# Performance work log

Measured on AMD Instinct MI355X. Metric: run time of the kernel, lower is better.

## Reference

```python
import jax, jax.numpy as jnp
import numpy as np

B, L = 8192, 2048

def setup_inputs() -> dict:
    key = jax.random.key(0)
    k1, k2 = jax.random.split(key)
    x = jax.random.normal(k1, (B, L), dtype=jnp.float32)
    y = jax.random.normal(k2, (B, L), dtype=jnp.float32)
    # MRS ppm axis is descending; GABA/Glx windows lie inside [1, 5] ppm
    ppm = jnp.linspace(5.0, 1.0, L, dtype=jnp.float32)
    return {"x": x, "ppm": ppm, "y": y}

def _bounds(ppm_np, lo, hi):
    # matches torch: start = amin(where(ppm <= hi)), stop = amax(where(ppm >= lo))
    mn = int(np.min(np.where(ppm_np <= hi)[0]))
    mx = int(np.max(np.where(ppm_np >= lo)[0]))
    return mn, mx

def _norm01(v):
    vmin = v.min(axis=-1, keepdims=True)
    vmax = v.max(axis=-1, keepdims=True)
    return (v - vmin) / (vmax - vmin)

def _pearson(a, b):
    # row-wise Pearson correlation == corrcoef(cat([a,b]))[0,1], batched over rows
    am = a - a.mean(axis=-1, keepdims=True)
    bm = b - b.mean(axis=-1, keepdims=True)
    return (am * bm).sum(-1) / jnp.sqrt((am * am).sum(-1) * (bm * bm).sum(-1))

def _loss(x, y, ppm_np):
    # ---- ShapeScoreLoss (gaba 2.8-3.2, glx 3.6-3.9, weights 0.6/0.4) ----
    g_lo, g_hi = _bounds(ppm_np, 2.8, 3.2)
    gaba_score = _pearson(_norm01(x[:, g_lo:g_hi]), _norm01(y[:, g_lo:g_hi]))
    s_lo, s_hi = _bounds(ppm_np, 3.6, 3.9)
    glx_score = _pearson(_norm01(x[:, s_lo:s_hi]), _norm01(y[:, s_lo:s_hi]))
    shape_loss = 1.0 - (0.6 * gaba_score + 0.4 * glx_score).mean()
    # ---- RangeMAELoss (gaba 2.8-3.2, glx 3.55-3.95, weights 6/3/1 over 10) ----
    r_lo, r_hi = _bounds(ppm_np, 3.55, 3.95)
    gaba_mae = jnp.abs(x[:, g_lo:g_hi] - y[:, g_lo:g_hi]).mean()
    glx_mae = jnp.abs(x[:, r_lo:r_hi] - y[:, r_lo:r_hi]).mean()
    global_mae = jnp.abs(x - y).mean()
    range_loss = (gaba_mae * 6.0 + glx_mae * 3.0 + global_mae) / 10.0
    return shape_loss + range_loss * 0.5

def reference(x, ppm, y):
    ppm_np = np.asarray(ppm)  # ppm is a fixed axis -> static slice bounds
    return _loss(x, y, ppm_np)
```

## Files before the change

### kernel.cpp

```cpp
#include <hip/hip_runtime.h>

#define L_COLS 2048

typedef float vf4 __attribute__((ext_vector_type(4)));

__device__ __forceinline__ float wave_red(float v) {
#pragma unroll
    for (int m = 32; m >= 1; m >>= 1) v += __shfl_xor(v, m, 64);
    return v;
}

__global__ __launch_bounds__(64) void init_kernel(const float* __restrict__ ppm,
                                                  float* __restrict__ acc,
                                                  int* __restrict__ ob) {
    const int lane = threadIdx.x;
    if (lane < 4) acc[lane] = 0.f;

    int mn0 = 0x7fffffff, mn1 = 0x7fffffff, mn2 = 0x7fffffff;
    int mx0 = -1, mx1 = -1, mx2 = -1;
    const vf4* __restrict__ p4 = (const vf4*)ppm;
#pragma unroll
    for (int k = 0; k < L_COLS / 256; ++k) {
        const int j = k * 64 + lane;
        const vf4 pv = p4[j];
        const float ps[4] = {pv.x, pv.y, pv.z, pv.w};
#pragma unroll
        for (int e = 0; e < 4; ++e) {
            const int c = 4 * j + e;
            const float p = ps[e];
            if (p <= 3.2f)  mn0 = min(mn0, c);
            if (p >= 2.8f)  mx0 = max(mx0, c);
            if (p <= 3.9f)  mn1 = min(mn1, c);
            if (p >= 3.6f)  mx1 = max(mx1, c);
            if (p <= 3.95f) mn2 = min(mn2, c);
            if (p >= 3.55f) mx2 = max(mx2, c);
        }
    }
#pragma unroll
    for (int m = 32; m >= 1; m >>= 1) {
        mn0 = min(mn0, __shfl_xor(mn0, m, 64));
        mx0 = max(mx0, __shfl_xor(mx0, m, 64));
        mn1 = min(mn1, __shfl_xor(mn1, m, 64));
        mx1 = max(mx1, __shfl_xor(mx1, m, 64));
        mn2 = min(mn2, __shfl_xor(mn2, m, 64));
        mx2 = max(mx2, __shfl_xor(mx2, m, 64));
    }
    if (lane == 0) {
        ob[0] = mn0; ob[1] = mx0;
        ob[2] = mn1; ob[3] = mx1;
        ob[4] = mn2; ob[5] = mx2;
    }
}

__global__ __launch_bounds__(256, 2) void loss_main(const float* __restrict__ x,
                                                    const float* __restrict__ y,
                                                    const int* __restrict__ ob,
                                                    float* __restrict__ acc) {
    const int lane = threadIdx.x & 63;
    const int wv   = threadIdx.x >> 6;
    const long row = (long)blockIdx.x * 4 + wv;

    const int g_lo = ob[0], g_hi = ob[1];
    const int s_lo = ob[2], s_hi = ob[3];
    const int r_lo = ob[4], r_hi = ob[5];
    const int lo_any = min(min(g_lo, s_lo), r_lo);
    const int hi_any = max(max(g_hi, s_hi), r_hi);

    const vf4* __restrict__ x4 = (const vf4*)(x + row * L_COLS);
    const vf4* __restrict__ y4 = (const vf4*)(y + row * L_COLS);

    vf4 xr[8], yr[8];
#pragma unroll
    for (int k = 0; k < 8; ++k) xr[k] = x4[k * 64 + lane];
#pragma unroll
    for (int k = 0; k < 8; ++k) yr[k] = y4[k * 64 + lane];

    float gl = 0.f;
    float a_sx = 0, a_sy = 0, a_xy = 0, a_xx = 0, a_yy = 0, a_mae = 0;
    float b_sx = 0, b_sy = 0, b_xy = 0, b_xx = 0, b_yy = 0;
    float r_mae = 0;

#pragma unroll
    for (int k = 0; k < 8; ++k) {
        const vf4 xv = xr[k];
        const vf4 yv = yr[k];
        const float d0 = fabsf(xv.x - yv.x), d1 = fabsf(xv.y - yv.y);
        const float d2 = fabsf(xv.z - yv.z), d3 = fabsf(xv.w - yv.w);
        gl += (d0 + d1) + (d2 + d3);

        if (k * 256 < hi_any && k * 256 + 256 > lo_any) {
            const float xs[4] = {xv.x, xv.y, xv.z, xv.w};
            const float ys[4] = {yv.x, yv.y, yv.z, yv.w};
            const float ds[4] = {d0, d1, d2, d3};
#pragma unroll
            for (int e = 0; e < 4; ++e) {
                const int c = k * 256 + 4 * lane + e;
                const float xe = xs[e], ye = ys[e];
                if (c >= g_lo && c < g_hi) {
                    a_sx += xe; a_sy += ye; a_xy += xe * ye;
                    a_xx += xe * xe; a_yy += ye * ye; a_mae += ds[e];
                }
                if (c >= s_lo && c < s_hi) {
                    b_sx += xe; b_sy += ye; b_xy += xe * ye;
                    b_xx += xe * xe; b_yy += ye * ye;
                }
                if (c >= r_lo && c < r_hi) r_mae += ds[e];
            }
        }
    }

    gl    = wave_red(gl);
    a_sx  = wave_red(a_sx);  a_sy = wave_red(a_sy);
    a_xy  = wave_red(a_xy);  a_xx = wave_red(a_xx);  a_yy = wave_red(a_yy);
    a_mae = wave_red(a_mae);
    b_sx  = wave_red(b_sx);  b_sy = wave_red(b_sy);
    b_xy  = wave_red(b_xy);  b_xx = wave_red(b_xx);  b_yy = wave_red(b_yy);
    r_mae = wave_red(r_mae);

    __shared__ float part[4][4];
    if (lane == 0) {
        const float ng = (float)(g_hi - g_lo);
        const float ns = (float)(s_hi - s_lo);
        const float covA = a_xy - a_sx * a_sy / ng;
        const float vAx  = a_xx - a_sx * a_sx / ng;
        const float vAy  = a_yy - a_sy * a_sy / ng;
        const float scoreA = covA * rsqrtf(vAx * vAy);
        const float covB = b_xy - b_sx * b_sy / ns;
        const float vBx  = b_xx - b_sx * b_sx / ns;
        const float vBy  = b_yy - b_sy * b_sy / ns;
        const float scoreB = covB * rsqrtf(vBx * vBy);
        part[wv][0] = 0.6f * scoreA + 0.4f * scoreB;
        part[wv][1] = a_mae;
        part[wv][2] = r_mae;
        part[wv][3] = gl;
    }
    __syncthreads();
    if (threadIdx.x < 4) {
        const float s = part[0][threadIdx.x] + part[1][threadIdx.x] +
                        part[2][threadIdx.x] + part[3][threadIdx.x];
        atomicAdd(&acc[threadIdx.x], s);
    }
}

__global__ void finalize_kernel(const float* __restrict__ acc, const int* __restrict__ ob,
                                int Brows, float* __restrict__ out) {
    const float ng = (float)(ob[1] - ob[0]);
    const float nr = (float)(ob[5] - ob[4]);
    const float Bf = (float)Brows;
    const float shape_loss = 1.f - acc[0] / Bf;
    const float gaba_mae = acc[1] / (Bf * ng);
    const float glx_mae  = acc[2] / (Bf * nr);
    const float glob_mae = acc[3] / (Bf * (float)L_COLS);
    const float range_loss = (gaba_mae * 6.f + glx_mae * 3.f + glob_mae) * 0.1f;
    out[0] = shape_loss + range_loss * 0.5f;
}

extern "C" void kernel_launch(void* const* d_in, const int* in_sizes, int n_in,
                              void* d_out, int out_size, void* d_ws, size_t ws_size,
                              hipStream_t stream) {
    const float* x   = (const float*)d_in[0];
    const float* ppm = (const float*)d_in[1];
    const float* y   = (const float*)d_in[2];
    const int L = in_sizes[1];
    const int Brows = in_sizes[0] / L;

    float* acc = (float*)d_ws;
    int*   ob  = (int*)((char*)d_ws + 64);

    init_kernel<<<1, 64, 0, stream>>>(ppm, acc, ob);
    loss_main<<<Brows / 4, 256, 0, stream>>>(x, y, ob, acc);
    finalize_kernel<<<1, 1, 0, stream>>>(acc, ob, Brows, (float*)d_out);
}
```

Baseline: 46.50 us.

## Process one row per block and spread atomics over multiple slots

Each row is now handled by a whole 256-thread block, with two vf4 loads per thread instead of one wave loading sixteen, and partial sums are combined through shared memory before the Pearson score is computed once per row. Atomic accumulation goes to 64 separate slot sets chosen by block index, and the finalize kernel reduces those slots with a wave. The aim is more memory parallelism, lower register pressure and less atomic contention. In exchange the grid has four times as many blocks, every thread evaluates the range predicates since the chunk-skip test is gone, and each block now pays a barrier and a serial single-thread final combine.

```diff
diff --git a/kernel.cpp b/kernel.cpp
--- a/kernel.cpp
+++ b/kernel.cpp
@@ -1,6 +1,7 @@
 #include <hip/hip_runtime.h>
 
 #define L_COLS 2048
+#define NSLOT 64
 
 typedef float vf4 __attribute__((ext_vector_type(4)));
 
@@ -14,7 +15,7 @@
                                                   float* __restrict__ acc,
                                                   int* __restrict__ ob) {
     const int lane = threadIdx.x;
-    if (lane < 4) acc[lane] = 0.f;
+    ((vf4*)acc)[lane] = (vf4){0.f, 0.f, 0.f, 0.f};
 
     int mn0 = 0x7fffffff, mn1 = 0x7fffffff, mn2 = 0x7fffffff;
     int mx0 = -1, mx1 = -1, mx2 = -1;
@@ -52,28 +53,26 @@
     }
 }
 
-__global__ __launch_bounds__(256, 2) void loss_main(const float* __restrict__ x,
-                                                    const float* __restrict__ y,
-                                                    const int* __restrict__ ob,
-                                                    float* __restrict__ acc) {
-    const int lane = threadIdx.x & 63;
-    const int wv   = threadIdx.x >> 6;
-    const long row = (long)blockIdx.x * 4 + wv;
+__global__ __launch_bounds__(256) void loss_main(const float* __restrict__ x,
+                                                 const float* __restrict__ y,
+                                                 const int* __restrict__ ob,
+                                                 float* __restrict__ acc) {
+    const int t    = threadIdx.x;
+    const int lane = t & 63;
+    const int wv   = t >> 6;
+    const long row = blockIdx.x;
 
     const int g_lo = ob[0], g_hi = ob[1];
     const int s_lo = ob[2], s_hi = ob[3];
     const int r_lo = ob[4], r_hi = ob[5];
-    const int lo_any = min(min(g_lo, s_lo), r_lo);
-    const int hi_any = max(max(g_hi, s_hi), r_hi);
 
     const vf4* __restrict__ x4 = (const vf4*)(x + row * L_COLS);
     const vf4* __restrict__ y4 = (const vf4*)(y + row * L_COLS);
 
-    vf4 xr[8], yr[8];
-#pragma unroll
-    for (int k = 0; k < 8; ++k) xr[k] = x4[k * 64 + lane];
-#pragma unroll
-    for (int k = 0; k < 8; ++k) yr[k] = y4[k * 64 + lane];
+    const vf4 xa = x4[t];
+    const vf4 xb = x4[256 + t];
+    const vf4 ya = y4[t];
+    const vf4 yb = y4[256 + t];
 
     float gl = 0.f;
     float a_sx = 0, a_sy = 0, a_xy = 0, a_xx = 0, a_yy = 0, a_mae = 0;
@@ -81,78 +80,89 @@
     float r_mae = 0;
 
 #pragma unroll
-    for (int k = 0; k < 8; ++k) {
-        const vf4 xv = xr[k];
-        const vf4 yv = yr[k];
-        const float d0 = fabsf(xv.x - yv.x), d1 = fabsf(xv.y - yv.y);
-        const float d2 = fabsf(xv.z - yv.z), d3 = fabsf(xv.w - yv.w);
-        gl += (d0 + d1) + (d2 + d3);
-
-        if (k * 256 < hi_any && k * 256 + 256 > lo_any) {
-            const float xs[4] = {xv.x, xv.y, xv.z, xv.w};
-            const float ys[4] = {yv.x, yv.y, yv.z, yv.w};
-            const float ds[4] = {d0, d1, d2, d3};
+    for (int h = 0; h < 2; ++h) {
+        const vf4 xv = h ? xb : xa;
+        const vf4 yv = h ? yb : ya;
+        const int c0 = h * 1024 + 4 * t;
+        const float xs[4] = {xv.x, xv.y, xv.z, xv.w};
+        const float ys[4] = {yv.x, yv.y, yv.z, yv.w};
 #pragma unroll
-            for (int e = 0; e < 4; ++e) {
-                const int c = k * 256 + 4 * lane + e;
-                const float xe = xs[e], ye = ys[e];
-                if (c >= g_lo && c < g_hi) {
-                    a_sx += xe; a_sy += ye; a_xy += xe * ye;
-                    a_xx += xe * xe; a_yy += ye * ye; a_mae += ds[e];
-                }
-                if (c >= s_lo && c < s_hi) {
-                    b_sx += xe; b_sy += ye; b_xy += xe * ye;
-                    b_xx += xe * xe; b_yy += ye * ye;
-                }
-                if (c >= r_lo && c < r_hi) r_mae += ds[e];
+        for (int e = 0; e < 4; ++e) {
+            const int c = c0 + e;
+            const float xe = xs[e], ye = ys[e];
+            const float d = fabsf(xe - ye);
+            gl += d;
+            if (c >= g_lo && c < g_hi) {
+                a_sx += xe; a_sy += ye; a_xy += xe * ye;
+                a_xx += xe * xe; a_yy += ye * ye; a_mae += d;
             }
+            if (c >= s_lo && c < s_hi) {
+                b_sx += xe; b_sy += ye; b_xy += xe * ye;
+                b_xx += xe * xe; b_yy += ye * ye;
+            }
+            if (c >= r_lo && c < r_hi) r_mae += d;
         }
     }
 
-    gl    = wave_red(gl);
-    a_sx  = wave_red(a_sx);  a_sy = wave_red(a_sy);
-    a_xy  = wave_red(a_xy);  a_xx = wave_red(a_xx);  a_yy = wave_red(a_yy);
-    a_mae = wave_red(a_mae);
-    b_sx  = wave_red(b_sx);  b_sy = wave_red(b_sy);
-    b_xy  = wave_red(b_xy);  b_xx = wave_red(b_xx);  b_yy = wave_red(b_yy);
-    r_mae = wave_red(r_mae);
+    float v0  = wave_red(gl);
+    float v1  = wave_red(a_sx), v2 = wave_red(a_sy), v3 = wave_red(a_xy);
+    float v4  = wave_red(a_xx), v5 = wave_red(a_yy), v6 = wave_red(a_mae);
+    float v7  = wave_red(b_sx), v8 = wave_red(b_sy), v9 = wave_red(b_xy);
+    float v10 = wave_red(b_xx), v11 = wave_red(b_yy);
+    float v12 = wave_red(r_mae);
 
-    __shared__ float part[4][4];
+    __shared__ float part[4][13];
     if (lane == 0) {
+        part[wv][0] = v0;  part[wv][1] = v1;  part[wv][2] = v2;
+        part[wv][3] = v3;  part[wv][4] = v4;  part[wv][5] = v5;
+        part[wv][6] = v6;  part[wv][7] = v7;  part[wv][8] = v8;
+        part[wv][9] = v9;  part[wv][10] = v10; part[wv][11] = v11;
+        part[wv][12] = v12;
+    }
+    __syncthreads();
+    if (t == 0) {
+        float s[13];
+#pragma unroll
+        for (int i = 0; i < 13; ++i)
+            s[i] = (part[0][i] + part[1][i]) + (part[2][i] + part[3][i]);
         const float ng = (float)(g_hi - g_lo);
         const float ns = (float)(s_hi - s_lo);
-        const float covA = a_xy - a_sx * a_sy / ng;
-        const float vAx  = a_xx - a_sx * a_sx / ng;
-        const float vAy  = a_yy - a_sy * a_sy / ng;
+        const float covA = s[3] - s[1] * s[2] / ng;
+        const float vAx  = s[4] - s[1] * s[1] / ng;
+        const float vAy  = s[5] - s[2] * s[2] / ng;
         const float scoreA = covA * rsqrtf(vAx * vAy);
-        const float covB = b_xy - b_sx * b_sy / ns;
-        const float vBx  = b_xx - b_sx * b_sx / ns;
-        const float vBy  = b_yy - b_sy * b_sy / ns;
+        const float covB = s[9] - s[7] * s[8] / ns;
+        const float vBx  = s[10] - s[7] * s[7] / ns;
+        const float vBy  = s[11] - s[8] * s[8] / ns;
         const float scoreB = covB * rsqrtf(vBx * vBy);
-        part[wv][0] = 0.6f * scoreA + 0.4f * scoreB;
-        part[wv][1] = a_mae;
-        part[wv][2] = r_mae;
-        part[wv][3] = gl;
-    }
-    __syncthreads();
-    if (threadIdx.x < 4) {
-        const float s = part[0][threadIdx.x] + part[1][threadIdx.x] +
-                        part[2][threadIdx.x] + part[3][threadIdx.x];
-        atomicAdd(&acc[threadIdx.x], s);
+        float* slot = acc + 4 * (blockIdx.x & (NSLOT - 1));
+        atomicAdd(&slot[0], 0.6f * scoreA + 0.4f * scoreB);
+        atomicAdd(&slot[1], s[6]);
+        atomicAdd(&slot[2], s[12]);
+        atomicAdd(&slot[3], s[0]);
     }
 }
 
-__global__ void finalize_kernel(const float* __restrict__ acc, const int* __restrict__ ob,
-                                int Brows, float* __restrict__ out) {
-    const float ng = (float)(ob[1] - ob[0]);
-    const float nr = (float)(ob[5] - ob[4]);
-    const float Bf = (float)Brows;
-    const float shape_loss = 1.f - acc[0] / Bf;
-    const float gaba_mae = acc[1] / (Bf * ng);
-    const float glx_mae  = acc[2] / (Bf * nr);
-    const float glob_mae = acc[3] / (Bf * (float)L_COLS);
-    const float range_loss = (gaba_mae * 6.f + glx_mae * 3.f + glob_mae) * 0.1f;
-    out[0] = shape_loss + range_loss * 0.5f;
+__global__ __launch_bounds__(64) void finalize_kernel(const float* __restrict__ acc,
+                                                      const int* __restrict__ ob,
+                                                      int Brows, float* __restrict__ out) {
+    const int lane = threadIdx.x;
+    vf4 v = ((const vf4*)acc)[lane];
+    v.x = wave_red(v.x);
+    v.y = wave_red(v.y);
+    v.z = wave_red(v.z);
+    v.w = wave_red(v.w);
+    if (lane == 0) {
+        const float ng = (float)(ob[1] - ob[0]);
+        const float nr = (float)(ob[5] - ob[4]);
+        const float Bf = (float)Brows;
+        const float shape_loss = 1.f - v.x / Bf;
+        const float gaba_mae = v.y / (Bf * ng);
+        const float glx_mae  = v.z / (Bf * nr);
+        const float glob_mae = v.w / (Bf * (float)L_COLS);
+        const float range_loss = (gaba_mae * 6.f + glx_mae * 3.f + glob_mae) * 0.1f;
+        out[0] = shape_loss + range_loss * 0.5f;
+    }
 }
 
 extern "C" void kernel_launch(void* const* d_in, const int* in_sizes, int n_in,
@@ -165,9 +175,9 @@
     const int Brows = in_sizes[0] / L;
 
     float* acc = (float*)d_ws;
-    int*   ob  = (int*)((char*)d_ws + 64);
+    int*   ob  = (int*)((char*)d_ws + 1024);
 
     init_kernel<<<1, 64, 0, stream>>>(ppm, acc, ob);
-    loss_main<<<Brows / 4, 256, 0, stream>>>(x, y, ob, acc);
-    finalize_kernel<<<1, 1, 0, stream>>>(acc, ob, Brows, (float*)d_out);
+    loss_main<<<Brows, 256, 0, stream>>>(x, y, ob, acc);
+    finalize_kernel<<<1, 64, 0, stream>>>(acc, ob, Brows, (float*)d_out);
 }
```

Result: slower. 72.89 us (+56.8%).
